# Optimization experiments

Hardware: AMD Instinct MI355X
Metric: run time of the kernel (lower is better)

The kernel has to match this reference:

```python
import jax, jax.numpy as jnp
import numpy as np

N_NODES = 100000
NUM_LAYER = 3
REG_WEIGHT = 1e-4


def setup_inputs() -> dict:
    key = jax.random.key(0)
    ks = jax.random.split(key, 6)
    E = 1280000
    B = 4096
    D = 64
    # xavier-uniform-like scale for embedding table
    emb_weight = jax.random.normal(ks[0], (N_NODES, D), dtype=jnp.float32) * 0.01
    src = jax.random.randint(ks[1], (E,), 0, N_NODES, dtype=jnp.int32)
    dst = jax.random.randint(ks[2], (E,), 0, N_NODES, dtype=jnp.int32)
    users = jax.random.randint(ks[3], (B,), 0, N_NODES, dtype=jnp.int32)
    pos = jax.random.randint(ks[4], (B,), 0, N_NODES, dtype=jnp.int32)
    neg = jax.random.randint(ks[5], (B,), 0, N_NODES, dtype=jnp.int32)
    return {"emb_weight": emb_weight, "src": src, "dst": dst,
            "users": users, "pos": pos, "neg": neg}


def _edge_norm(src, dst):
    # DGL norm(): d = sum of edge mask (ones) per dst node; adj_e = d[src]^-0.5 * d[dst]^-0.5
    ones = jnp.ones(src.shape[0], dtype=jnp.float32)
    deg = jax.ops.segment_sum(ones, dst, num_segments=N_NODES)
    dinv = jnp.where(deg > 0, deg ** -0.5, 0.0)  # inf -> 0 handling
    return dinv[src] * dinv[dst]  # [E]


def _propagate(emb_weight, src, dst, adj):
    # LightGCN propagation: h_{l+1}[v] = sum_{(u->v)} adj_e * h_l[u]
    h = emb_weight
    layers = [h]
    for _ in range(NUM_LAYER):
        m = h[src] * adj[:, None]                    # [E, D] gather + edge weight
        h = jax.ops.segment_sum(m, dst, num_segments=N_NODES)  # [N, D] scatter-sum
        layers.append(h)
    return jnp.mean(jnp.stack(layers, axis=1), axis=1)  # mean over L+1 layers


def reference(emb_weight, src, dst, users, pos, neg):
    adj = _edge_norm(src, dst)
    all_emb = _propagate(emb_weight, src, dst, adj)

    u_e, p_e, n_e = all_emb[users], all_emb[pos], all_emb[neg]
    u0, p0, n0 = emb_weight[users], emb_weight[pos], emb_weight[neg]

    B = users.shape[0]
    reg_loss = 0.5 * (jnp.sum(u0 ** 2) + jnp.sum(p0 ** 2) + jnp.sum(n0 ** 2)) / B
    reg_loss = reg_loss * REG_WEIGHT

    pos_scores = jnp.sum(u_e * p_e, axis=1)
    neg_scores = jnp.sum(u_e * n_e, axis=1)
    loss_emb = jnp.mean(jax.nn.softplus(neg_scores - pos_scores))

    loss = loss_emb + reg_loss
    return loss, loss_emb, reg_loss
```

## Files before the change

### kernel.cpp

```cpp
#include <hip/hip_runtime.h>
#include <hip/hip_fp8.h>
#include <math.h>

#define N_NODES 100000
#define DIM 64
#define NUM_LAYER 3
#define BATCH 4096
#define REG_WEIGHT 1e-4f
#define NBUCKET 391
#define STAGE_CAP 4096
#define CURPAD 16
#define H_SCALE 64.0f
#define H_INV_SCALE (1.0f / 64.0f)

__device__ unsigned char g_hf8[2][(size_t)N_NODES * DIM];
__device__ float g_sums[(size_t)3 * BATCH * DIM];
__device__ int   g_row_ptr[N_NODES + 1];
__device__ float g_dinv[N_NODES];
__device__ int   g_bcur[NBUCKET * CURPAD];
__device__ int   g_bbase[NBUCKET];
__device__ int2  g_stage[NBUCKET * STAGE_CAP];
__device__ int2  g_csr[1280000];
__device__ float g_part_sp[BATCH];
__device__ float g_part_rg[BATCH];

__device__ inline float fp8_to_f32(unsigned int v) {
    __hip_fp8_e4m3 t; t.__x = (__hip_fp8_storage_t)(v & 0xFF); return (float)t;
}
__device__ inline unsigned int f32_to_fp8(float f) {
    __hip_fp8_e4m3 t(f); return (unsigned int)t.__x;
}

__global__ void init_bcur() {
    int i = blockIdx.x * blockDim.x + threadIdx.x;
    if (i < NBUCKET) g_bcur[i * CURPAD] = i * STAGE_CAP;
}

#define EDGES_PER_THREAD 8
__global__ void __launch_bounds__(1024) stage_buckets(const int* __restrict__ src,
                                                      const int* __restrict__ dst, int E) {
    __shared__ int h[NBUCKET];
    __shared__ int cur[NBUCKET];
    int tid = threadIdx.x;
    int base = blockIdx.x * (1024 * EDGES_PER_THREAD);
    for (int i = tid; i < NBUCKET; i += 1024) h[i] = 0;
    __syncthreads();
    int myd[EDGES_PER_THREAD], mys[EDGES_PER_THREAD];
    #pragma unroll
    for (int k = 0; k < EDGES_PER_THREAD; ++k) {
        int e = base + k * 1024 + tid;
        if (e < E) {
            myd[k] = dst[e]; mys[k] = src[e];
            atomicAdd(&h[myd[k] >> 8], 1);
        } else myd[k] = -1;
    }
    __syncthreads();
    for (int i = tid; i < NBUCKET; i += 1024) {
        int c = h[i];
        cur[i] = c ? atomicAdd(&g_bcur[i * CURPAD], c) : 0;
    }
    __syncthreads();
    #pragma unroll
    for (int k = 0; k < EDGES_PER_THREAD; ++k) {
        if (myd[k] >= 0) {
            int p = atomicAdd(&cur[myd[k] >> 8], 1);
            g_stage[p] = make_int2(mys[k], myd[k]);
        }
    }
}

__global__ void btotals_scan(int E) {
    __shared__ int sm[512];
    int t = threadIdx.x;
    int c = (t < NBUCKET) ? (g_bcur[t * CURPAD] - t * STAGE_CAP) : 0;
    sm[t] = c;
    __syncthreads();
    for (int off = 1; off < 512; off <<= 1) {
        int x = (t >= off) ? sm[t - off] : 0;
        __syncthreads();
        sm[t] += x;
        __syncthreads();
    }
    if (t < NBUCKET) g_bbase[t] = sm[t] - c;
    if (t == 0) g_row_ptr[N_NODES] = E;
}

__global__ void bucket_finalize() {
    __shared__ int lh[256];
    __shared__ int sc[256];
    int b = blockIdx.x, t = threadIdx.x;
    int cnt  = g_bcur[b * CURPAD] - b * STAGE_CAP;
    int sbeg = b * STAGE_CAP;
    lh[t] = 0;
    __syncthreads();
    for (int k = t; k < cnt; k += 256)
        atomicAdd(&lh[g_stage[sbeg + k].y & 255], 1);
    __syncthreads();
    int v = lh[t];
    sc[t] = v;
    __syncthreads();
    for (int off = 1; off < 256; off <<= 1) {
        int x = (t >= off) ? sc[t - off] : 0;
        __syncthreads();
        sc[t] += x;
        __syncthreads();
    }
    int node = (b << 8) + t;
    if (node < N_NODES) {
        g_row_ptr[node] = g_bbase[b] + sc[t] - v;
        g_dinv[node]    = (v > 0) ? rsqrtf((float)v) : 0.0f;
    }
}

__global__ void bucket_place() {
    __shared__ int cur[256];
    int b = blockIdx.x, t = threadIdx.x;
    int cnt  = g_bcur[b * CURPAD] - b * STAGE_CAP;
    int sbeg = b * STAGE_CAP;
    int node = (b << 8) + t;
    cur[t] = (node < N_NODES) ? g_row_ptr[node] : 0;
    __syncthreads();
    for (int k = t; k < cnt; k += 256) {
        int2 sd = g_stage[sbeg + k];
        int pos = atomicAdd(&cur[sd.y & 255], 1);
        float w = g_dinv[sd.x] * g_dinv[sd.y];
        g_csr[pos] = make_int2(sd.x, __float_as_int(w));
    }
}

__global__ void emb_to_fp8(const float* __restrict__ emb, unsigned char* __restrict__ hf) {
    size_t i = (size_t)blockIdx.x * blockDim.x + threadIdx.x;
    size_t stride = (size_t)gridDim.x * blockDim.x;
    for (size_t k = i; k < (size_t)N_NODES * DIM; k += stride)
        hf[k] = (unsigned char)f32_to_fp8(emb[k] * H_SCALE);
}

__global__ void pull_layer_fp8(const unsigned char* __restrict__ h,
                               unsigned char* __restrict__ hn) {
    int wid  = (blockIdx.x * blockDim.x + threadIdx.x) >> 6;
    int lane = threadIdx.x & 63;
    if (wid >= N_NODES) return;
    int g  = lane >> 4;
    int li = lane & 15;
    int beg = g_row_ptr[wid], end = g_row_ptr[wid + 1];
    float a0 = 0.f, a1 = 0.f, a2 = 0.f, a3 = 0.f;
    for (int base = beg; base < end; base += 64) {
        int k = base + lane;
        int s = 0; float w = 0.0f;
        if (k < end) { int2 ew = g_csr[k]; s = ew.x; w = __int_as_float(ew.y); }
        int cnt = min(64, end - base);
        for (int j = 0; j < cnt; j += 8) {
            int   sA = __shfl(s, j + g);
            float wA = __shfl(w, j + g);
            int   sB = __shfl(s, j + 4 + g);
            float wB = __shfl(w, j + 4 + g);
            unsigned int dA = *(const unsigned int*)(h + (size_t)sA * DIM + li * 4);
            unsigned int dB = *(const unsigned int*)(h + (size_t)sB * DIM + li * 4);
            a0 = fmaf(wA, fp8_to_f32(dA),       a0);
            a1 = fmaf(wA, fp8_to_f32(dA >> 8),  a1);
            a2 = fmaf(wA, fp8_to_f32(dA >> 16), a2);
            a3 = fmaf(wA, fp8_to_f32(dA >> 24), a3);
            a0 = fmaf(wB, fp8_to_f32(dB),       a0);
            a1 = fmaf(wB, fp8_to_f32(dB >> 8),  a1);
            a2 = fmaf(wB, fp8_to_f32(dB >> 16), a2);
            a3 = fmaf(wB, fp8_to_f32(dB >> 24), a3);
        }
    }
    #pragma unroll
    for (int off = 16; off < 64; off <<= 1) {
        a0 += __shfl_xor(a0, off);
        a1 += __shfl_xor(a1, off);
        a2 += __shfl_xor(a2, off);
        a3 += __shfl_xor(a3, off);
    }
    if (lane < 16) {
        unsigned int outw = f32_to_fp8(a0) | (f32_to_fp8(a1) << 8) |
                            (f32_to_fp8(a2) << 16) | (f32_to_fp8(a3) << 24);
        *(unsigned int*)(hn + (size_t)wid * DIM + li * 4) = outw;
    }
}

__global__ void pull_sampled(const unsigned char* __restrict__ h,
                             const int* __restrict__ users, const int* __restrict__ pos,
                             const int* __restrict__ neg) {
    int wid  = (blockIdx.x * blockDim.x + threadIdx.x) >> 6;
    int lane = threadIdx.x & 63;
    if (wid >= 3 * BATCH) return;
    int which = wid / BATCH;
    int i     = wid - which * BATCH;
    const int* idx = (which == 0) ? users : ((which == 1) ? pos : neg);
    int node = idx[i];
    int g  = lane >> 4;
    int li = lane & 15;
    int beg = g_row_ptr[node], end = g_row_ptr[node + 1];
    float a0 = 0.f, a1 = 0.f, a2 = 0.f, a3 = 0.f;
    for (int base = beg; base < end; base += 64) {
        int k = base + lane;
        int s = 0; float w = 0.0f;
        if (k < end) { int2 ew = g_csr[k]; s = ew.x; w = __int_as_float(ew.y); }
        int cnt = min(64, end - base);
        for (int j = 0; j < cnt; j += 8) {
            int   sA = __shfl(s, j + g);
            float wA = __shfl(w, j + g);
            int   sB = __shfl(s, j + 4 + g);
            float wB = __shfl(w, j + 4 + g);
            unsigned int dA = *(const unsigned int*)(h + (size_t)sA * DIM + li * 4);
            unsigned int dB = *(const unsigned int*)(h + (size_t)sB * DIM + li * 4);
            a0 = fmaf(wA, fp8_to_f32(dA),       a0);
            a1 = fmaf(wA, fp8_to_f32(dA >> 8),  a1);
            a2 = fmaf(wA, fp8_to_f32(dA >> 16), a2);
            a3 = fmaf(wA, fp8_to_f32(dA >> 24), a3);
            a0 = fmaf(wB, fp8_to_f32(dB),       a0);
            a1 = fmaf(wB, fp8_to_f32(dB >> 8),  a1);
            a2 = fmaf(wB, fp8_to_f32(dB >> 16), a2);
            a3 = fmaf(wB, fp8_to_f32(dB >> 24), a3);
        }
    }
    #pragma unroll
    for (int off = 16; off < 64; off <<= 1) {
        a0 += __shfl_xor(a0, off);
        a1 += __shfl_xor(a1, off);
        a2 += __shfl_xor(a2, off);
        a3 += __shfl_xor(a3, off);
    }
    if (lane < 16) {
        unsigned int dn = *(const unsigned int*)(h + (size_t)node * DIM + li * 4);
        float* sp = &g_sums[(size_t)wid * DIM + li * 4];
        sp[0] += (a0 + fp8_to_f32(dn))       * H_INV_SCALE;
        sp[1] += (a1 + fp8_to_f32(dn >> 8))  * H_INV_SCALE;
        sp[2] += (a2 + fp8_to_f32(dn >> 16)) * H_INV_SCALE;
        sp[3] += (a3 + fp8_to_f32(dn >> 24)) * H_INV_SCALE;
    }
}

__global__ void gather_acc_f32(const float* __restrict__ h,
                               const int* __restrict__ users, const int* __restrict__ pos,
                               const int* __restrict__ neg) {
    int wid  = (blockIdx.x * blockDim.x + threadIdx.x) >> 6;
    int lane = threadIdx.x & 63;
    if (wid >= 3 * BATCH) return;
    int which = wid / BATCH;
    int i     = wid - which * BATCH;
    const int* idx = (which == 0) ? users : ((which == 1) ? pos : neg);
    int node = idx[i];
    g_sums[(size_t)wid * DIM + lane] = h[(size_t)node * DIM + lane];
}

__global__ void gather_acc_fp8(const unsigned char* __restrict__ h,
                               const int* __restrict__ users, const int* __restrict__ pos,
                               const int* __restrict__ neg) {
    int wid  = (blockIdx.x * blockDim.x + threadIdx.x) >> 6;
    int lane = threadIdx.x & 63;
    if (wid >= 3 * BATCH) return;
    int which = wid / BATCH;
    int i     = wid - which * BATCH;
    const int* idx = (which == 0) ? users : ((which == 1) ? pos : neg);
    int node = idx[i];
    g_sums[(size_t)wid * DIM + lane] += fp8_to_f32(h[(size_t)node * DIM + lane]) * H_INV_SCALE;
}

__global__ void score_reduce(const float* __restrict__ emb,
                             const int* __restrict__ users, const int* __restrict__ pos,
                             const int* __restrict__ neg) {
    int wid  = (blockIdx.x * blockDim.x + threadIdx.x) >> 6;
    int lane = threadIdx.x & 63;
    if (wid >= BATCH) return;
    float u = 0.25f * g_sums[(size_t)wid * DIM + lane];
    float p = 0.25f * g_sums[(size_t)(BATCH + wid) * DIM + lane];
    float n = 0.25f * g_sums[(size_t)(2 * BATCH + wid) * DIM + lane];
    float ps = u * p;
    float ns = u * n;
    float u0 = emb[(size_t)users[wid] * DIM + lane];
    float p0 = emb[(size_t)pos[wid]   * DIM + lane];
    float n0 = emb[(size_t)neg[wid]   * DIM + lane];
    float rg = u0 * u0 + p0 * p0 + n0 * n0;
    #pragma unroll
    for (int off = 32; off > 0; off >>= 1) {
        ps += __shfl_down(ps, off);
        ns += __shfl_down(ns, off);
        rg += __shfl_down(rg, off);
    }
    if (lane == 0) {
        float x  = ns - ps;
        float sp = fmaxf(x, 0.0f) + log1pf(expf(-fabsf(x)));
        g_part_sp[wid] = sp;
        g_part_rg[wid] = rg;
    }
}

__global__ void final_reduce(float* __restrict__ out) {
    __shared__ float s_sp[256], s_rg[256];
    int t = threadIdx.x;
    float sp = 0.0f, rg = 0.0f;
    for (int i = t; i < BATCH; i += 256) { sp += g_part_sp[i]; rg += g_part_rg[i]; }
    s_sp[t] = sp; s_rg[t] = rg;
    __syncthreads();
    for (int off = 128; off > 0; off >>= 1) {
        if (t < off) { s_sp[t] += s_sp[t + off]; s_rg[t] += s_rg[t + off]; }
        __syncthreads();
    }
    if (t == 0) {
        float loss_emb = s_sp[0] / (float)BATCH;
        float reg      = 0.5f * s_rg[0] / (float)BATCH * REG_WEIGHT;
        out[0] = loss_emb + reg;
        out[1] = loss_emb;
        out[2] = reg;
    }
}

extern "C" void kernel_launch(void* const* d_in, const int* in_sizes, int n_in,
                              void* d_out, int out_size, void* d_ws, size_t ws_size,
                              hipStream_t stream) {
    const float* emb   = (const float*)d_in[0];
    const int*   src   = (const int*)d_in[1];
    const int*   dst   = (const int*)d_in[2];
    const int*   users = (const int*)d_in[3];
    const int*   pos   = (const int*)d_in[4];
    const int*   neg   = (const int*)d_in[5];
    const int E = in_sizes[1];
    float* out = (float*)d_out;

    unsigned char* hf_a;  hipGetSymbolAddress((void**)&hf_a, HIP_SYMBOL(g_hf8));
    unsigned char* hf_b = hf_a + (size_t)N_NODES * DIM;

    init_bcur<<<(NBUCKET + 255) / 256, 256, 0, stream>>>();

    const int STAGE_BLOCKS = (E + 1024 * EDGES_PER_THREAD - 1) / (1024 * EDGES_PER_THREAD);
    stage_buckets<<<STAGE_BLOCKS, 1024, 0, stream>>>(src, dst, E);
    btotals_scan<<<1, 512, 0, stream>>>(E);
    bucket_finalize<<<NBUCKET, 256, 0, stream>>>();
    bucket_place<<<NBUCKET, 256, 0, stream>>>();

    emb_to_fp8<<<2048, 256, 0, stream>>>(emb, hf_a);

    gather_acc_f32<<<(3 * BATCH * 64 + 255) / 256, 256, 0, stream>>>(emb, users, pos, neg);

    pull_layer_fp8<<<(N_NODES * 64 + 255) / 256, 256, 0, stream>>>(hf_a, hf_b);
    gather_acc_fp8<<<(3 * BATCH * 64 + 255) / 256, 256, 0, stream>>>(hf_b, users, pos, neg);

    pull_layer_fp8<<<(N_NODES * 64 + 255) / 256, 256, 0, stream>>>(hf_b, hf_a);

    pull_sampled<<<(3 * BATCH * 64 + 255) / 256, 256, 0, stream>>>(hf_a, users, pos, neg);

    score_reduce<<<(BATCH * 64 + 255) / 256, 256, 0, stream>>>(emb, users, pos, neg);
    final_reduce<<<1, 256, 0, stream>>>(out);
}
```

Before: 225.6 us.

## Fuse setup kernels, pack staged edges into 32-bit, merge bucket scan into finalize

Merges init_bcur, the fp8 conversion and the f32 sample gather into one prelude kernel, and writes packed 4-byte fp8 words instead of single bytes. Staged edges are stored as one 32-bit word (src<<8 | dst low byte) instead of an int2, which halves staging traffic. The separate bucket-totals scan kernel is folded into bucket_finalize, where every block redoes the 391-entry scan. The goal is to cut launch count and memory traffic in the preprocessing phase. The packing assumes src < 2^24, which holds for 100000 nodes.

```diff
diff --git a/kernel.cpp b/kernel.cpp
--- a/kernel.cpp
+++ b/kernel.cpp
@@ -18,8 +18,7 @@
 __device__ int   g_row_ptr[N_NODES + 1];
 __device__ float g_dinv[N_NODES];
 __device__ int   g_bcur[NBUCKET * CURPAD];
-__device__ int   g_bbase[NBUCKET];
-__device__ int2  g_stage[NBUCKET * STAGE_CAP];
+__device__ unsigned int g_stage[NBUCKET * STAGE_CAP];
 __device__ int2  g_csr[1280000];
 __device__ float g_part_sp[BATCH];
 __device__ float g_part_rg[BATCH];
@@ -31,9 +30,25 @@
     __hip_fp8_e4m3 t(f); return (unsigned int)t.__x;
 }
 
-__global__ void init_bcur() {
+__global__ void prelude(const float* __restrict__ emb,
+                        const int* __restrict__ users, const int* __restrict__ pos,
+                        const int* __restrict__ neg) {
     int i = blockIdx.x * blockDim.x + threadIdx.x;
-    if (i < NBUCKET) g_bcur[i * CURPAD] = i * STAGE_CAP;
+    int stride = gridDim.x * blockDim.x;
+    for (int k = i; k < NBUCKET; k += stride) g_bcur[k * CURPAD] = k * STAGE_CAP;
+    const int NW = N_NODES * DIM / 4;
+    unsigned int* hw = (unsigned int*)g_hf8[0];
+    for (int k = i; k < NW; k += stride) {
+        const float* e = emb + (size_t)k * 4;
+        hw[k] = f32_to_fp8(e[0] * H_SCALE)         | (f32_to_fp8(e[1] * H_SCALE) << 8) |
+                (f32_to_fp8(e[2] * H_SCALE) << 16) | (f32_to_fp8(e[3] * H_SCALE) << 24);
+    }
+    for (int k = i; k < 3 * BATCH * DIM; k += stride) {
+        int wid = k >> 6, lane = k & 63;
+        int which = wid / BATCH, s = wid - which * BATCH;
+        const int* idx = (which == 0) ? users : ((which == 1) ? pos : neg);
+        g_sums[k] = emb[(size_t)idx[s] * DIM + lane];
+    }
 }
 
 #define EDGES_PER_THREAD 8
@@ -64,51 +79,48 @@
     for (int k = 0; k < EDGES_PER_THREAD; ++k) {
         if (myd[k] >= 0) {
             int p = atomicAdd(&cur[myd[k] >> 8], 1);
-            g_stage[p] = make_int2(mys[k], myd[k]);
+            g_stage[p] = (unsigned int)((mys[k] << 8) | (myd[k] & 255));
         }
     }
 }
 
-__global__ void btotals_scan(int E) {
-    __shared__ int sm[512];
-    int t = threadIdx.x;
+__global__ void __launch_bounds__(512) bucket_finalize() {
+    __shared__ int cs[512];
+    __shared__ int lh[256], sc[256];
+    int b = blockIdx.x, t = threadIdx.x;
     int c = (t < NBUCKET) ? (g_bcur[t * CURPAD] - t * STAGE_CAP) : 0;
-    sm[t] = c;
+    cs[t] = c;
     __syncthreads();
     for (int off = 1; off < 512; off <<= 1) {
-        int x = (t >= off) ? sm[t - off] : 0;
-        __syncthreads();
-        sm[t] += x;
-        __syncthreads();
-    }
-    if (t < NBUCKET) g_bbase[t] = sm[t] - c;
-    if (t == 0) g_row_ptr[N_NODES] = E;
-}
-
-__global__ void bucket_finalize() {
-    __shared__ int lh[256];
-    __shared__ int sc[256];
-    int b = blockIdx.x, t = threadIdx.x;
-    int cnt  = g_bcur[b * CURPAD] - b * STAGE_CAP;
+        int x = (t >= off) ? cs[t - off] : 0;
+        __syncthreads();
+        cs[t] += x;
+        __syncthreads();
+    }
+    int mybase = (b > 0) ? cs[b - 1] : 0;
+    int cnt    = cs[b] - mybase;
+    if (b == 0 && t == 0) g_row_ptr[N_NODES] = cs[NBUCKET - 1];
     int sbeg = b * STAGE_CAP;
-    lh[t] = 0;
-    __syncthreads();
-    for (int k = t; k < cnt; k += 256)
-        atomicAdd(&lh[g_stage[sbeg + k].y & 255], 1);
-    __syncthreads();
-    int v = lh[t];
-    sc[t] = v;
+    if (t < 256) lh[t] = 0;
+    __syncthreads();
+    for (int k = t; k < cnt; k += 512)
+        atomicAdd(&lh[g_stage[sbeg + k] & 255], 1);
+    __syncthreads();
+    int v = 0;
+    if (t < 256) { v = lh[t]; sc[t] = v; }
     __syncthreads();
     for (int off = 1; off < 256; off <<= 1) {
-        int x = (t >= off) ? sc[t - off] : 0;
-        __syncthreads();
-        sc[t] += x;
-        __syncthreads();
-    }
-    int node = (b << 8) + t;
-    if (node < N_NODES) {
-        g_row_ptr[node] = g_bbase[b] + sc[t] - v;
-        g_dinv[node]    = (v > 0) ? rsqrtf((float)v) : 0.0f;
+        int x = (t >= off && t < 256) ? sc[t - off] : 0;
+        __syncthreads();
+        if (t < 256) sc[t] += x;
+        __syncthreads();
+    }
+    if (t < 256) {
+        int node = (b << 8) + t;
+        if (node < N_NODES) {
+            g_row_ptr[node] = mybase + sc[t] - v;
+            g_dinv[node]    = (v > 0) ? rsqrtf((float)v) : 0.0f;
+        }
     }
 }
 
@@ -121,18 +133,14 @@
     cur[t] = (node < N_NODES) ? g_row_ptr[node] : 0;
     __syncthreads();
     for (int k = t; k < cnt; k += 256) {
-        int2 sd = g_stage[sbeg + k];
-        int pos = atomicAdd(&cur[sd.y & 255], 1);
-        float w = g_dinv[sd.x] * g_dinv[sd.y];
-        g_csr[pos] = make_int2(sd.x, __float_as_int(w));
-    }
-}
-
-__global__ void emb_to_fp8(const float* __restrict__ emb, unsigned char* __restrict__ hf) {
-    size_t i = (size_t)blockIdx.x * blockDim.x + threadIdx.x;
-    size_t stride = (size_t)gridDim.x * blockDim.x;
-    for (size_t k = i; k < (size_t)N_NODES * DIM; k += stride)
-        hf[k] = (unsigned char)f32_to_fp8(emb[k] * H_SCALE);
+        unsigned int e = g_stage[sbeg + k];
+        int dl = e & 255;
+        int s  = (int)(e >> 8);
+        int pos = atomicAdd(&cur[dl], 1);
+        int d = (b << 8) + dl;
+        float w = g_dinv[s] * g_dinv[d];
+        g_csr[pos] = make_int2(s, __float_as_int(w));
+    }
 }
 
 __global__ void pull_layer_fp8(const unsigned char* __restrict__ h,
@@ -233,19 +241,6 @@
     }
 }
 
-__global__ void gather_acc_f32(const float* __restrict__ h,
-                               const int* __restrict__ users, const int* __restrict__ pos,
-                               const int* __restrict__ neg) {
-    int wid  = (blockIdx.x * blockDim.x + threadIdx.x) >> 6;
-    int lane = threadIdx.x & 63;
-    if (wid >= 3 * BATCH) return;
-    int which = wid / BATCH;
-    int i     = wid - which * BATCH;
-    const int* idx = (which == 0) ? users : ((which == 1) ? pos : neg);
-    int node = idx[i];
-    g_sums[(size_t)wid * DIM + lane] = h[(size_t)node * DIM + lane];
-}
-
 __global__ void gather_acc_fp8(const unsigned char* __restrict__ h,
                                const int* __restrict__ users, const int* __restrict__ pos,
                                const int* __restrict__ neg) {
@@ -323,17 +318,12 @@
     unsigned char* hf_a;  hipGetSymbolAddress((void**)&hf_a, HIP_SYMBOL(g_hf8));
     unsigned char* hf_b = hf_a + (size_t)N_NODES * DIM;
 
-    init_bcur<<<(NBUCKET + 255) / 256, 256, 0, stream>>>();
+    prelude<<<1024, 256, 0, stream>>>(emb, users, pos, neg);
 
     const int STAGE_BLOCKS = (E + 1024 * EDGES_PER_THREAD - 1) / (1024 * EDGES_PER_THREAD);
     stage_buckets<<<STAGE_BLOCKS, 1024, 0, stream>>>(src, dst, E);
-    btotals_scan<<<1, 512, 0, stream>>>(E);
-    bucket_finalize<<<NBUCKET, 256, 0, stream>>>();
+    bucket_finalize<<<NBUCKET, 512, 0, stream>>>();
     bucket_place<<<NBUCKET, 256, 0, stream>>>();
-
-    emb_to_fp8<<<2048, 256, 0, stream>>>(emb, hf_a);
-
-    gather_acc_f32<<<(3 * BATCH * 64 + 255) / 256, 256, 0, stream>>>(emb, users, pos, neg);
 
     pull_layer_fp8<<<(N_NODES * 64 + 255) / 256, 256, 0, stream>>>(hf_a, hf_b);
     gather_acc_fp8<<<(3 * BATCH * 64 + 255) / 256, 256, 0, stream>>>(hf_b, users, pos, neg);
```

Measured after the change: 211.2 us. 6.4% less time.
